# Optimization experiments

Measured on AMD Instinct MI355X. Metric: run time of the kernel, lower is better.

## Reference

```python
import jax, jax.numpy as jnp
import numpy as np

B, N, D, H, E = 4, 1024, 512, 8, 5
HD = D // H  # head_dim = 64


def _xavier(k, shape):
    fan_out, fan_in = shape
    s = (2.0 / (fan_in + fan_out)) ** 0.5
    return jax.random.normal(k, shape, jnp.float32) * s


def setup_inputs() -> dict:
    key = jax.random.key(0)
    ks = jax.random.split(key, 7)
    x = jax.random.normal(ks[0], (B, N, D), jnp.float32)
    edge_features = jax.random.normal(ks[1], (B, N, N, E), jnp.float32)
    node_mask = jax.random.randint(ks[2], (B, N), 0, 2).astype(bool)
    w_qkv = _xavier(ks[3], (3 * D, D))
    w_ep = _xavier(ks[4], (H, E))
    w_eg = _xavier(ks[5], (H, E))
    b_eg = jnp.zeros((H,), jnp.float32)
    w_proj = _xavier(ks[6], (D, D))
    b_proj = jnp.zeros((D,), jnp.float32)
    return {"x": x, "edge_features": edge_features, "node_mask": node_mask,
            "w_qkv": w_qkv, "w_ep": w_ep, "w_eg": w_eg, "b_eg": b_eg,
            "w_proj": w_proj, "b_proj": b_proj}


def reference(x, edge_features, node_mask, w_qkv, w_ep, w_eg, b_eg, w_proj, b_proj):
    b, n, d = x.shape
    scale = HD ** -0.5
    # qkv projection (torch Linear: y = x @ W^T), split into q,k,v (b,H,n,HD)
    qkv = (x @ w_qkv.T).reshape(b, n, 3, H, HD)
    qkv = jnp.transpose(qkv, (2, 0, 3, 1, 4))
    q, k, v = qkv[0], qkv[1], qkv[2]
    # attention scores (b,H,n,n)
    scores = jnp.einsum('bhnd,bhmd->bhnm', q, k) * scale
    # edge bias and sigmoid gate, (b,n,n,E) @ (E,H) -> (b,H,n,n)
    edge_bias = jnp.einsum('bnme,he->bhnm', edge_features, w_ep)
    edge_gates = jax.nn.sigmoid(
        jnp.einsum('bnme,he->bhnm', edge_features, w_eg) + b_eg[None, :, None, None])
    scores = scores + edge_gates * edge_bias
    # pairwise valid mask, broadcast over heads
    m = node_mask[:, None, :, None] & node_mask[:, None, None, :]  # (b,1,n,n)
    scores = jnp.where(m, scores, -jnp.inf)
    row_valid = jnp.any(m, axis=-1)  # (b,1,n)
    scores = jnp.where(row_valid[..., None], scores, 0.0)
    attn = jax.nn.softmax(scores, axis=-1)
    out = jnp.einsum('bhnm,bhmd->bhnd', attn, v)
    out = jnp.transpose(out, (0, 2, 1, 3)).reshape(b, n, d)
    return out @ w_proj.T + b_proj
```

## Files before the change

kernel.cpp:

```cpp
#include <hip/hip_runtime.h>
#include <hip/hip_bf16.h>

#define Bb 4
#define Nn 1024
#define Dd 512
#define Hh 8
#define Ee 5
#define HDd 64

typedef unsigned int u32_t;
typedef unsigned short u16_t;
typedef short s16x8 __attribute__((ext_vector_type(8)));
typedef float f32x4 __attribute__((ext_vector_type(4)));

#define MFMA(a, b, c) __builtin_amdgcn_mfma_f32_16x16x32_bf16((a), (b), (c), 0, 0, 0)

__device__ __forceinline__ void lds_barrier() {
    asm volatile("s_waitcnt lgkmcnt(0)" ::: "memory");
    __builtin_amdgcn_s_barrier();
    asm volatile("" ::: "memory");
}

__device__ __forceinline__ u32_t pack32(float x) {
    u32_t u = __float_as_uint(x);
    u32_t hi = u & 0xffff0000u;
    float rem = x - __uint_as_float(hi);
    u32_t r = __float_as_uint(rem);
    u32_t lo = (r + 0x7fffu + ((r >> 16) & 1u)) >> 16;
    return hi | (lo & 0xffffu);
}

__device__ __forceinline__ void unpk8(uint4 A, uint4 B, s16x8& h, s16x8& l) {
    union { u16_t u[8]; s16x8 v; } H, L;
    u32_t a[8] = {A.x, A.y, A.z, A.w, B.x, B.y, B.z, B.w};
    #pragma unroll
    for (int i = 0; i < 8; i++) { H.u[i] = (u16_t)(a[i] >> 16); L.u[i] = (u16_t)(a[i] & 0xffffu); }
    h = H.v; l = L.v;
}

__device__ __forceinline__ void split4(uint4 A, uint2& hi, uint2& lo) {
    hi.x = (A.x >> 16) | (A.y & 0xffff0000u);
    hi.y = (A.z >> 16) | (A.w & 0xffff0000u);
    lo.x = (A.x & 0xffffu) | (A.y << 16);
    lo.y = (A.z & 0xffffu) | (A.w << 16);
}

__device__ __forceinline__ void stage16(uint4 A0, uint4 A1, uint4 A2, uint4 A3,
                                        u16_t* dh, u16_t* dl) {
    uint2 h0, l0, h1, l1, h2, l2, h3, l3;
    split4(A0, h0, l0); split4(A1, h1, l1); split4(A2, h2, l2); split4(A3, h3, l3);
    *(uint4*)(dh + 0) = make_uint4(h0.x, h0.y, h1.x, h1.y);
    *(uint4*)(dh + 8) = make_uint4(h2.x, h2.y, h3.x, h3.y);
    *(uint4*)(dl + 0) = make_uint4(l0.x, l0.y, l1.x, l1.y);
    *(uint4*)(dl + 8) = make_uint4(l2.x, l2.y, l3.x, l3.y);
}

__global__ __launch_bounds__(256) void pack_prep(const float* __restrict__ x,
                                                 const float* __restrict__ wq,
                                                 const float* __restrict__ wpj,
                                                 const void* __restrict__ msk,
                                                 u32_t* __restrict__ xp,
                                                 u32_t* __restrict__ wqp,
                                                 u32_t* __restrict__ wpp,
                                                 int* __restrict__ mw,
                                                 int* __restrict__ anyB) {
    __shared__ int notint;
    __shared__ int ab[Bb];
    const int tid = threadIdx.x;
    if (blockIdx.x == 1024) {
        if (tid == 0) notint = 0;
        if (tid < Bb) ab[tid] = 0;
        __syncthreads();
        const u32_t* wp = (const u32_t*)msk;
        int bad = 0;
        for (int i = tid; i < 1024; i += 256) bad |= (wp[i] > 1u);
        if (bad) atomicOr(&notint, 1);
        __syncthreads();
        const int isbyte = notint;
        const unsigned char* bp = (const unsigned char*)msk;
        for (int i = tid; i < Bb * Nn; i += 256) {
            const int v = isbyte ? (bp[i] != 0) : (wp[i] != 0);
            mw[i] = v;
            if (v) atomicOr(&ab[i >> 10], 1);
        }
        __syncthreads();
        if (tid < Bb) anyB[tid] = ab[tid];
        return;
    }
    const int gt = blockIdx.x * 256 + tid;
    const int gs = 1024 * 256;
    const float4* xs = (const float4*)x;
    uint4* xd = (uint4*)xp;
    for (int i = gt; i < (Bb * Nn * Dd) / 4; i += gs) {
        float4 v = xs[i];
        xd[i] = make_uint4(pack32(v.x), pack32(v.y), pack32(v.z), pack32(v.w));
    }
    const float4* qs = (const float4*)wq;
    uint4* qd = (uint4*)wqp;
    for (int i = gt; i < (3 * Dd * Dd) / 4; i += gs) {
        float4 v = qs[i];
        qd[i] = make_uint4(pack32(v.x), pack32(v.y), pack32(v.z), pack32(v.w));
    }
    const float4* ps = (const float4*)wpj;
    uint4* pd = (uint4*)wpp;
    for (int i = gt; i < (Dd * Dd) / 4; i += gs) {
        float4 v = ps[i];
        pd[i] = make_uint4(pack32(v.x), pack32(v.y), pack32(v.z), pack32(v.w));
    }
}

__global__ __launch_bounds__(256) void qkv_mfma(const u32_t* __restrict__ xp,
                                                const u32_t* __restrict__ wp,
                                                u32_t* __restrict__ q32,
                                                u32_t* __restrict__ k32,
                                                u32_t* __restrict__ v32) {
    __shared__ __align__(16) u16_t Xh[64 * 72], Xl[64 * 72];
    __shared__ __align__(16) u16_t Wh[64 * 72], Wl[64 * 72];
    const int tid = threadIdx.x;
    const int wv = tid >> 6, lane = tid & 63, lm = lane & 15, quad = lane >> 4;
    const int m0 = blockIdx.y * 64, c0 = blockIdx.x * 64;
    const int row = tid >> 2, dq = tid & 3;
    const uint4* x4 = (const uint4*)xp;
    const uint4* w4 = (const uint4*)wp;

    const size_t xb0 = (size_t)(m0 + row) * 128 + dq * 4;
    const size_t wb0 = (size_t)(c0 + row) * 128 + dq * 4;
    uint4 xa0 = x4[xb0 + 0], xa1 = x4[xb0 + 1], xa2 = x4[xb0 + 2], xa3 = x4[xb0 + 3];
    uint4 wa0 = w4[wb0 + 0], wa1 = w4[wb0 + 1], wa2 = w4[wb0 + 2], wa3 = w4[wb0 + 3];

    f32x4 acc[4];
    #pragma unroll
    for (int nt = 0; nt < 4; nt++) acc[nt] = {0.f, 0.f, 0.f, 0.f};

    for (int kt = 0; kt < 8; kt++) {
        lds_barrier();
        stage16(xa0, xa1, xa2, xa3, &Xh[row * 72 + dq * 16], &Xl[row * 72 + dq * 16]);
        stage16(wa0, wa1, wa2, wa3, &Wh[row * 72 + dq * 16], &Wl[row * 72 + dq * 16]);
        const int ktn = (kt < 7) ? kt + 1 : 7;
        xa0 = x4[xb0 + ktn * 16 + 0]; xa1 = x4[xb0 + ktn * 16 + 1];
        xa2 = x4[xb0 + ktn * 16 + 2]; xa3 = x4[xb0 + ktn * 16 + 3];
        wa0 = w4[wb0 + ktn * 16 + 0]; wa1 = w4[wb0 + ktn * 16 + 1];
        wa2 = w4[wb0 + ktn * 16 + 2]; wa3 = w4[wb0 + ktn * 16 + 3];
        lds_barrier();
        s16x8 ah[2], al[2];
        #pragma unroll
        for (int ks = 0; ks < 2; ks++) {
            ah[ks] = *(const s16x8*)&Xh[(16 * wv + lm) * 72 + ks * 32 + quad * 8];
            al[ks] = *(const s16x8*)&Xl[(16 * wv + lm) * 72 + ks * 32 + quad * 8];
        }
        #pragma unroll
        for (int nt = 0; nt < 4; nt++) {
            #pragma unroll
            for (int ks = 0; ks < 2; ks++) {
                s16x8 bh = *(const s16x8*)&Wh[(16 * nt + lm) * 72 + ks * 32 + quad * 8];
                s16x8 bl = *(const s16x8*)&Wl[(16 * nt + lm) * 72 + ks * 32 + quad * 8];
                acc[nt] = MFMA(ah[ks], bh, acc[nt]);
                acc[nt] = MFMA(ah[ks], bl, acc[nt]);
                acc[nt] = MFMA(al[ks], bh, acc[nt]);
            }
        }
    }
    #pragma unroll
    for (int nt = 0; nt < 4; nt++) {
        const int c = c0 + 16 * nt + lm;
        const int s = c >> 9, hd = c & 511, h = hd >> 6, d = hd & 63;
        u32_t* dst = (s == 0) ? q32 : (s == 1) ? k32 : v32;
        #pragma unroll
        for (int r = 0; r < 4; r++) {
            const int m = m0 + 16 * wv + 4 * quad + r;
            const int b = m >> 10, n = m & (Nn - 1);
            dst[(((size_t)b * Hh + h) * Nn + n) * HDd + d] = pack32(acc[nt][r]);
        }
    }
}

__global__ __launch_bounds__(256, 2) void attn_mfma(const u32_t* __restrict__ q32,
                                                    const u32_t* __restrict__ k32,
                                                    const u32_t* __restrict__ v32,
                                                    const float* __restrict__ ef,
                                                    const int* __restrict__ mw,
                                                    const int* __restrict__ anyB,
                                                    const float* __restrict__ wep,
                                                    const float* __restrict__ weg,
                                                    const float* __restrict__ beg,
                                                    u32_t* __restrict__ aoutp) {
    __shared__ __align__(16) u16_t Qh[64 * 72], Ql[64 * 72];
    __shared__ __align__(16) u16_t Kh[64 * 72], Kl[64 * 72];
    __shared__ __align__(16) u16_t VTh[64 * 88], VTl[64 * 88];
    __shared__ __align__(16) u32_t Ppk[64 * 68];

    const int tid = threadIdx.x;
    const int wv = tid >> 6, lane = tid & 63, lm = lane & 15, quad = lane >> 4;
    const int i0 = blockIdx.x * 64;
    const int h  = blockIdx.y;
    const int b  = blockIdx.z;
    const int row = tid >> 2, dq = tid & 3;
    const int jg = tid >> 4, dc = tid & 15;

    const uint4* qg4 = (const uint4*)(q32 + (((size_t)b * Hh + h) * Nn + i0) * HDd);
    const uint4* kg4 = (const uint4*)(k32 + (((size_t)b * Hh + h) * Nn) * HDd);
    const uint4* vg4 = (const uint4*)(v32 + (((size_t)b * Hh + h) * Nn) * HDd);
    const int* mwB = mw + b * Nn;

    const size_t qb = (size_t)row * 16 + dq * 4;
    uint4 qA0 = qg4[qb + 0], qA1 = qg4[qb + 1], qA2 = qg4[qb + 2], qA3 = qg4[qb + 3];
    uint4 kr0 = kg4[qb + 0], kr1 = kg4[qb + 1], kr2 = kg4[qb + 2], kr3 = kg4[qb + 3];
    uint4 vr0 = vg4[(4 * jg + 0) * 16 + dc], vr1 = vg4[(4 * jg + 1) * 16 + dc],
          vr2 = vg4[(4 * jg + 2) * 16 + dc], vr3 = vg4[(4 * jg + 3) * 16 + dc];

    const int i_sm = i0 + 16 * wv + lm;
    const float* efL = ef + ((size_t)(b * Nn + i_sm) * Nn + 4 * quad) * Ee;
    int4 mj4[4];
    float4 er4[4][5];
    #pragma unroll
    for (int jn = 0; jn < 4; jn++) {
        mj4[jn] = *(const int4*)&mwB[16 * jn + 4 * quad];
        const float4* p4 = (const float4*)(efL + (size_t)(16 * jn) * Ee);
        #pragma unroll
        for (int c = 0; c < 5; c++) er4[jn][c] = p4[c];
    }

    const float wp0 = wep[h*Ee+0], wp1 = wep[h*Ee+1], wp2 = wep[h*Ee+2],
                wp3 = wep[h*Ee+3], wp4 = wep[h*Ee+4];
    const float wg0 = weg[h*Ee+0], wg1 = weg[h*Ee+1], wg2 = weg[h*Ee+2],
                wg3 = weg[h*Ee+3], wg4 = weg[h*Ee+4];
    const float bgs = beg[h];
    const int anyb = anyB[b];
    const int rvs = anyb && mwB[i_sm];

    stage16(qA0, qA1, qA2, qA3, &Qh[row * 72 + dq * 16], &Ql[row * 72 + dq * 16]);
    lds_barrier();
    s16x8 qh[2], ql[2];
    #pragma unroll
    for (int ks = 0; ks < 2; ks++) {
        qh[ks] = *(const s16x8*)&Qh[(16 * wv + lm) * 72 + ks * 32 + quad * 8];
        ql[ks] = *(const s16x8*)&Ql[(16 * wv + lm) * 72 + ks * 32 + quad * 8];
    }

    float m_ = -1e30f, l_ = 0.f;
    f32x4 accO[4];
    #pragma unroll
    for (int dn = 0; dn < 4; dn++) accO[dn] = {0.f, 0.f, 0.f, 0.f};
    const int xk = 8 * (lm & 3);

    for (int jt = 0; jt < Nn / 64; jt++) {
        const int jtn = (jt + 1 < Nn / 64) ? jt + 1 : Nn / 64 - 1;
        const int j0n = jtn * 64;

        lds_barrier();

        stage16(kr0, kr1, kr2, kr3, &Kh[row * 72 + dq * 16], &Kl[row * 72 + dq * 16]);
        {
            u32_t r0[4] = {vr0.x, vr0.y, vr0.z, vr0.w};
            u32_t r1[4] = {vr1.x, vr1.y, vr1.z, vr1.w};
            u32_t r2[4] = {vr2.x, vr2.y, vr2.z, vr2.w};
            u32_t r3[4] = {vr3.x, vr3.y, vr3.z, vr3.w};
            #pragma unroll
            for (int c = 0; c < 4; c++) {
                const int d = 4 * dc + c;
                uint2 hi, lo;
                hi.x = (r0[c] >> 16) | (r1[c] & 0xffff0000u);
                hi.y = (r2[c] >> 16) | (r3[c] & 0xffff0000u);
                lo.x = (r0[c] & 0xffffu) | (r1[c] << 16);
                lo.y = (r2[c] & 0xffffu) | (r3[c] << 16);
                *(uint2*)&VTh[d * 88 + 4 * jg] = hi;
                *(uint2*)&VTl[d * 88 + 4 * jg] = lo;
            }
        }
        {
            const size_t kbn = (size_t)(j0n + row) * 16 + dq * 4;
            kr0 = kg4[kbn + 0]; kr1 = kg4[kbn + 1]; kr2 = kg4[kbn + 2]; kr3 = kg4[kbn + 3];
            vr0 = vg4[(j0n + 4 * jg + 0) * 16 + dc];
            vr1 = vg4[(j0n + 4 * jg + 1) * 16 + dc];
            vr2 = vg4[(j0n + 4 * jg + 2) * 16 + dc];
            vr3 = vg4[(j0n + 4 * jg + 3) * 16 + dc];
        }

        lds_barrier();

        f32x4 Sp[4];
        #pragma unroll
        for (int jn = 0; jn < 4; jn++) {
            f32x4 s = {0.f, 0.f, 0.f, 0.f};
            #pragma unroll
            for (int ks = 0; ks < 2; ks++) {
                s16x8 kh = *(const s16x8*)&Kh[(16 * jn + lm) * 72 + ks * 32 + quad * 8];
                s16x8 kl = *(const s16x8*)&Kl[(16 * jn + lm) * 72 + ks * 32 + quad * 8];
                s = MFMA(kh, qh[ks], s);
                s = MFMA(kh, ql[ks], s);
                s = MFMA(kl, qh[ks], s);
            }
            Sp[jn] = s;
        }

        float pp[4][4];
        #pragma unroll
        for (int jn = 0; jn < 4; jn++) {
            const int mjv[4] = {mj4[jn].x, mj4[jn].y, mj4[jn].z, mj4[jn].w};
            #pragma unroll
            for (int r = 0; r < 4; r++) {
                const int f = r * 5;
                const float e0 = er4[jn][(f+0)>>2][(f+0)&3];
                const float e1 = er4[jn][(f+1)>>2][(f+1)&3];
                const float e2 = er4[jn][(f+2)>>2][(f+2)&3];
                const float e3 = er4[jn][(f+3)>>2][(f+3)&3];
                const float e4 = er4[jn][(f+4)>>2][(f+4)&3];
                const float bias = fmaf(e0, wp0, fmaf(e1, wp1, fmaf(e2, wp2, fmaf(e3, wp3, e4 * wp4))));
                const float gv = fmaf(e0, wg0, fmaf(e1, wg1, fmaf(e2, wg2, fmaf(e3, wg3, fmaf(e4, wg4, bgs)))));
                const float gate = __builtin_amdgcn_rcpf(1.f + __expf(-gv));
                const float val = fmaf(Sp[jn][r], 0.125f, gate * bias);
                pp[jn][r] = rvs ? (mjv[r] ? val : -1e30f) : 0.f;
            }
        }
        #pragma unroll
        for (int jn = 0; jn < 4; jn++) {
            mj4[jn] = *(const int4*)&mwB[j0n + 16 * jn + 4 * quad];
            const float4* p4 = (const float4*)(efL + (size_t)(j0n + 16 * jn) * Ee);
            #pragma unroll
            for (int c = 0; c < 5; c++) er4[jn][c] = p4[c];
        }

        float tmax = fmaxf(fmaxf(fmaxf(pp[0][0], pp[0][1]), fmaxf(pp[0][2], pp[0][3])),
                           fmaxf(fmaxf(pp[1][0], pp[1][1]), fmaxf(pp[1][2], pp[1][3])));
        tmax = fmaxf(tmax,
               fmaxf(fmaxf(fmaxf(pp[2][0], pp[2][1]), fmaxf(pp[2][2], pp[2][3])),
                     fmaxf(fmaxf(pp[3][0], pp[3][1]), fmaxf(pp[3][2], pp[3][3]))));
        tmax = fmaxf(tmax, __shfl_xor(tmax, 16));
        tmax = fmaxf(tmax, __shfl_xor(tmax, 32));
        const float mnew = fmaxf(m_, tmax);
        const float alpha = __expf(m_ - mnew);
        float ps = 0.f;
        #pragma unroll
        for (int jn = 0; jn < 4; jn++)
            #pragma unroll
            for (int r = 0; r < 4; r++) { pp[jn][r] = __expf(pp[jn][r] - mnew); ps += pp[jn][r]; }
        ps += __shfl_xor(ps, 16);
        ps += __shfl_xor(ps, 32);
        m_ = mnew;
        l_ = l_ * alpha + ps;
        float a4[4];
        #pragma unroll
        for (int r = 0; r < 4; r++) a4[r] = __shfl(alpha, 4 * quad + r);
        #pragma unroll
        for (int dn = 0; dn < 4; dn++)
            #pragma unroll
            for (int r = 0; r < 4; r++) accO[dn][r] *= a4[r];

        #pragma unroll
        for (int jn = 0; jn < 4; jn++) {
            #pragma unroll
            for (int p = 0; p < 2; p++) {
                const int col = (16 * jn + 4 * quad + 2 * p) ^ xk;
                *(uint2*)&Ppk[(16 * wv + lm) * 68 + col] =
                    make_uint2(pack32(pp[jn][2 * p]), pack32(pp[jn][2 * p + 1]));
            }
        }

        s16x8 ph[2], pl[2];
        #pragma unroll
        for (int ks2 = 0; ks2 < 2; ks2++) {
            const int off = (16 * wv + lm) * 68 + ((ks2 * 32 + quad * 8) ^ xk);
            uint4 A = *(const uint4*)&Ppk[off];
            uint4 B2 = *(const uint4*)&Ppk[off + 4];
            unpk8(A, B2, ph[ks2], pl[ks2]);
        }
        #pragma unroll
        for (int dn = 0; dn < 4; dn++) {
            f32x4 c = accO[dn];
            #pragma unroll
            for (int ks2 = 0; ks2 < 2; ks2++) {
                s16x8 vh = *(const s16x8*)&VTh[(16 * dn + lm) * 88 + ks2 * 32 + quad * 8];
                s16x8 vl = *(const s16x8*)&VTl[(16 * dn + lm) * 88 + ks2 * 32 + quad * 8];
                c = MFMA(ph[ks2], vh, c);
                c = MFMA(ph[ks2], vl, c);
                c = MFMA(pl[ks2], vh, c);
            }
            accO[dn] = c;
        }
    }

    float linv[4];
    #pragma unroll
    for (int r = 0; r < 4; r++) linv[r] = __builtin_amdgcn_rcpf(__shfl(l_, 4 * quad + r));
    #pragma unroll
    for (int r = 0; r < 4; r++) {
        const int i = i0 + 16 * wv + 4 * quad + r;
        #pragma unroll
        for (int dn = 0; dn < 4; dn++)
            aoutp[(size_t)(b * Nn + i) * Dd + h * HDd + 16 * dn + lm] = pack32(accO[dn][r] * linv[r]);
    }
}

__global__ __launch_bounds__(256) void out_mfma(const u32_t* __restrict__ ap,
                                                const u32_t* __restrict__ wp,
                                                const float* __restrict__ bias,
                                                float* __restrict__ out) {
    __shared__ __align__(16) u16_t Xh[64 * 72], Xl[64 * 72];
    __shared__ __align__(16) u16_t Wh[64 * 72], Wl[64 * 72];
    const int tid = threadIdx.x;
    const int wv = tid >> 6, lane = tid & 63, lm = lane & 15, quad = lane >> 4;
    const int m0 = blockIdx.y * 64, c0 = blockIdx.x * 64;
    const int row = tid >> 2, dq = tid & 3;
    const uint4* a4 = (const uint4*)ap;
    const uint4* w4 = (const uint4*)wp;

    const size_t ab0 = (size_t)(m0 + row) * 128 + dq * 4;
    const size_t wb0 = (size_t)(c0 + row) * 128 + dq * 4;
    uint4 xa0 = a4[ab0 + 0], xa1 = a4[ab0 + 1], xa2 = a4[ab0 + 2], xa3 = a4[ab0 + 3];
    uint4 wa0 = w4[wb0 + 0], wa1 = w4[wb0 + 1], wa2 = w4[wb0 + 2], wa3 = w4[wb0 + 3];

    f32x4 acc[4];
    #pragma unroll
    for (int nt = 0; nt < 4; nt++) acc[nt] = {0.f, 0.f, 0.f, 0.f};

    for (int kt = 0; kt < 8; kt++) {
        lds_barrier();
        stage16(xa0, xa1, xa2, xa3, &Xh[row * 72 + dq * 16], &Xl[row * 72 + dq * 16]);
        stage16(wa0, wa1, wa2, wa3, &Wh[row * 72 + dq * 16], &Wl[row * 72 + dq * 16]);
        const int ktn = (kt < 7) ? kt + 1 : 7;
        xa0 = a4[ab0 + ktn * 16 + 0]; xa1 = a4[ab0 + ktn * 16 + 1];
        xa2 = a4[ab0 + ktn * 16 + 2]; xa3 = a4[ab0 + ktn * 16 + 3];
        wa0 = w4[wb0 + ktn * 16 + 0]; wa1 = w4[wb0 + ktn * 16 + 1];
        wa2 = w4[wb0 + ktn * 16 + 2]; wa3 = w4[wb0 + ktn * 16 + 3];
        lds_barrier();
        s16x8 ah[2], al[2];
        #pragma unroll
        for (int ks = 0; ks < 2; ks++) {
            ah[ks] = *(const s16x8*)&Xh[(16 * wv + lm) * 72 + ks * 32 + quad * 8];
            al[ks] = *(const s16x8*)&Xl[(16 * wv + lm) * 72 + ks * 32 + quad * 8];
        }
        #pragma unroll
        for (int nt = 0; nt < 4; nt++) {
            #pragma unroll
            for (int ks = 0; ks < 2; ks++) {
                s16x8 bh = *(const s16x8*)&Wh[(16 * nt + lm) * 72 + ks * 32 + quad * 8];
                s16x8 bl = *(const s16x8*)&Wl[(16 * nt + lm) * 72 + ks * 32 + quad * 8];
                acc[nt] = MFMA(ah[ks], bh, acc[nt]);
                acc[nt] = MFMA(ah[ks], bl, acc[nt]);
                acc[nt] = MFMA(al[ks], bh, acc[nt]);
            }
        }
    }
    #pragma unroll
    for (int nt = 0; nt < 4; nt++) {
        const int c = c0 + 16 * nt + lm;
        const float bc = bias[c];
        #pragma unroll
        for (int r = 0; r < 4; r++) {
            const int m = m0 + 16 * wv + 4 * quad + r;
            out[(size_t)m * Dd + c] = acc[nt][r] + bc;
        }
    }
}

extern "C" void kernel_launch(void* const* d_in, const int* in_sizes, int n_in,
                              void* d_out, int out_size, void* d_ws, size_t ws_size,
                              hipStream_t stream) {
    const float* x    = (const float*)d_in[0];
    const float* ef   = (const float*)d_in[1];
    const void*  msk  = d_in[2];
    const float* wqkv = (const float*)d_in[3];
    const float* wep  = (const float*)d_in[4];
    const float* weg  = (const float*)d_in[5];
    const float* beg  = (const float*)d_in[6];
    const float* wpj  = (const float*)d_in[7];
    const float* bpj  = (const float*)d_in[8];
    float* out = (float*)d_out;

    int* mw   = (int*)d_ws;
    int* anyB = mw + Bb * Nn;
    u32_t* q32 = (u32_t*)(anyB + 16);
    const size_t per = (size_t)Bb * Hh * Nn * HDd;
    u32_t* k32 = q32 + per;
    u32_t* v32 = k32 + per;
    u32_t* aop = v32 + per;
    u32_t* xp  = aop + (size_t)Bb * Nn * Dd;
    u32_t* wqp = xp + (size_t)Bb * Nn * Dd;
    u32_t* wpp = wqp + (size_t)3 * Dd * Dd;

    pack_prep<<<1025, 256, 0, stream>>>(x, wqkv, wpj, msk, xp, wqp, wpp, mw, anyB);
    qkv_mfma<<<dim3(24, 64), 256, 0, stream>>>(xp, wqp, q32, k32, v32);
    attn_mfma<<<dim3(Nn / 64, Hh, Bb), 256, 0, stream>>>(q32, k32, v32, ef, mw, anyB,
                                                         wep, weg, beg, aop);
    out_mfma<<<dim3(8, 64), 256, 0, stream>>>(aop, wpp, bpj, out);
}
```

Baseline: 310.8 us.

## Bit-pack node mask, load Q directly to registers, widen V transpose stores

The node mask is packed into 32-bit bitmasks, so the attention kernel reads one uint2 per tile instead of four int4 loads per lane. The Q tile no longer goes through LDS: each lane loads its own Q row fragment and splits it into hi/lo bf16 halves in registers, which removes the Qh/Ql shared arrays and a barrier. The V transpose staging now gathers 8 rows with uint2 loads and writes 16-byte vectors to LDS instead of 8-byte ones. These changes cut LDS footprint and memory traffic at the cost of more uncoalesced per-lane Q loads and extra registers.

```diff
diff --git a/kernel.cpp b/kernel.cpp
--- a/kernel.cpp
+++ b/kernel.cpp
@@ -55,6 +55,9 @@
     *(uint4*)(dl + 8) = make_uint4(l2.x, l2.y, l3.x, l3.y);
 }
 
+#define HHW(a, b) (((a) >> 16) | ((b) & 0xffff0000u))
+#define LLW(a, b) (((a) & 0xffffu) | ((b) << 16))
+
 __global__ __launch_bounds__(256) void pack_prep(const float* __restrict__ x,
                                                  const float* __restrict__ wq,
                                                  const float* __restrict__ wpj,
@@ -62,7 +65,7 @@
                                                  u32_t* __restrict__ xp,
                                                  u32_t* __restrict__ wqp,
                                                  u32_t* __restrict__ wpp,
-                                                 int* __restrict__ mw,
+                                                 u32_t* __restrict__ mb,
                                                  int* __restrict__ anyB) {
     __shared__ int notint;
     __shared__ int ab[Bb];
@@ -78,10 +81,15 @@
         __syncthreads();
         const int isbyte = notint;
         const unsigned char* bp = (const unsigned char*)msk;
-        for (int i = tid; i < Bb * Nn; i += 256) {
-            const int v = isbyte ? (bp[i] != 0) : (wp[i] != 0);
-            mw[i] = v;
-            if (v) atomicOr(&ab[i >> 10], 1);
+        if (tid < 128) {
+            u32_t wbits = 0;
+            for (int k = 0; k < 32; k++) {
+                const int i = tid * 32 + k;
+                const int v = isbyte ? (bp[i] != 0) : (wp[i] != 0);
+                wbits |= (u32_t)v << k;
+            }
+            mb[tid] = wbits;
+            if (wbits) atomicOr(&ab[tid >> 5], 1);
         }
         __syncthreads();
         if (tid < Bb) anyB[tid] = ab[tid];
@@ -178,13 +186,12 @@
                                                     const u32_t* __restrict__ k32,
                                                     const u32_t* __restrict__ v32,
                                                     const float* __restrict__ ef,
-                                                    const int* __restrict__ mw,
+                                                    const u32_t* __restrict__ mb,
                                                     const int* __restrict__ anyB,
                                                     const float* __restrict__ wep,
                                                     const float* __restrict__ weg,
                                                     const float* __restrict__ beg,
                                                     u32_t* __restrict__ aoutp) {
-    __shared__ __align__(16) u16_t Qh[64 * 72], Ql[64 * 72];
     __shared__ __align__(16) u16_t Kh[64 * 72], Kl[64 * 72];
     __shared__ __align__(16) u16_t VTh[64 * 88], VTl[64 * 88];
     __shared__ __align__(16) u32_t Ppk[64 * 68];
@@ -195,26 +202,31 @@
     const int h  = blockIdx.y;
     const int b  = blockIdx.z;
     const int row = tid >> 2, dq = tid & 3;
-    const int jg = tid >> 4, dc = tid & 15;
-
-    const uint4* qg4 = (const uint4*)(q32 + (((size_t)b * Hh + h) * Nn + i0) * HDd);
+    const int jo = tid >> 5, dch = tid & 31;
+
     const uint4* kg4 = (const uint4*)(k32 + (((size_t)b * Hh + h) * Nn) * HDd);
-    const uint4* vg4 = (const uint4*)(v32 + (((size_t)b * Hh + h) * Nn) * HDd);
-    const int* mwB = mw + b * Nn;
-
-    const size_t qb = (size_t)row * 16 + dq * 4;
-    uint4 qA0 = qg4[qb + 0], qA1 = qg4[qb + 1], qA2 = qg4[qb + 2], qA3 = qg4[qb + 3];
-    uint4 kr0 = kg4[qb + 0], kr1 = kg4[qb + 1], kr2 = kg4[qb + 2], kr3 = kg4[qb + 3];
-    uint4 vr0 = vg4[(4 * jg + 0) * 16 + dc], vr1 = vg4[(4 * jg + 1) * 16 + dc],
-          vr2 = vg4[(4 * jg + 2) * 16 + dc], vr3 = vg4[(4 * jg + 3) * 16 + dc];
+    const uint2* vg2 = (const uint2*)(v32 + (((size_t)b * Hh + h) * Nn) * HDd);
+    const u32_t* mbB = mb + b * 32;
 
     const int i_sm = i0 + 16 * wv + lm;
+
+    const u32_t* qrow = q32 + (((size_t)b * Hh + h) * Nn + i_sm) * HDd;
+    uint4 qA0 = *(const uint4*)&qrow[quad * 8];
+    uint4 qB0 = *(const uint4*)&qrow[quad * 8 + 4];
+    uint4 qA1 = *(const uint4*)&qrow[32 + quad * 8];
+    uint4 qB1 = *(const uint4*)&qrow[32 + quad * 8 + 4];
+    const size_t kb0 = (size_t)row * 16 + dq * 4;
+    uint4 kr0 = kg4[kb0 + 0], kr1 = kg4[kb0 + 1], kr2 = kg4[kb0 + 2], kr3 = kg4[kb0 + 3];
+    uint2 vq0 = vg2[(8 * jo + 0) * 32 + dch], vq1 = vg2[(8 * jo + 1) * 32 + dch],
+          vq2 = vg2[(8 * jo + 2) * 32 + dch], vq3 = vg2[(8 * jo + 3) * 32 + dch],
+          vq4 = vg2[(8 * jo + 4) * 32 + dch], vq5 = vg2[(8 * jo + 5) * 32 + dch],
+          vq6 = vg2[(8 * jo + 6) * 32 + dch], vq7 = vg2[(8 * jo + 7) * 32 + dch];
+
     const float* efL = ef + ((size_t)(b * Nn + i_sm) * Nn + 4 * quad) * Ee;
-    int4 mj4[4];
+    uint2 mwc = *(const uint2*)&mbB[0];
     float4 er4[4][5];
     #pragma unroll
     for (int jn = 0; jn < 4; jn++) {
-        mj4[jn] = *(const int4*)&mwB[16 * jn + 4 * quad];
         const float4* p4 = (const float4*)(efL + (size_t)(16 * jn) * Ee);
         #pragma unroll
         for (int c = 0; c < 5; c++) er4[jn][c] = p4[c];
@@ -226,16 +238,11 @@
                 wg3 = weg[h*Ee+3], wg4 = weg[h*Ee+4];
     const float bgs = beg[h];
     const int anyb = anyB[b];
-    const int rvs = anyb && mwB[i_sm];
-
-    stage16(qA0, qA1, qA2, qA3, &Qh[row * 72 + dq * 16], &Ql[row * 72 + dq * 16]);
-    lds_barrier();
+    const int rvs = anyb && ((mbB[i_sm >> 5] >> (i_sm & 31)) & 1);
+
     s16x8 qh[2], ql[2];
-    #pragma unroll
-    for (int ks = 0; ks < 2; ks++) {
-        qh[ks] = *(const s16x8*)&Qh[(16 * wv + lm) * 72 + ks * 32 + quad * 8];
-        ql[ks] = *(const s16x8*)&Ql[(16 * wv + lm) * 72 + ks * 32 + quad * 8];
-    }
+    unpk8(qA0, qB0, qh[0], ql[0]);
+    unpk8(qA1, qB1, qh[1], ql[1]);
 
     float m_ = -1e30f, l_ = 0.f;
     f32x4 accO[4];
@@ -251,29 +258,31 @@
 
         stage16(kr0, kr1, kr2, kr3, &Kh[row * 72 + dq * 16], &Kl[row * 72 + dq * 16]);
         {
-            u32_t r0[4] = {vr0.x, vr0.y, vr0.z, vr0.w};
-            u32_t r1[4] = {vr1.x, vr1.y, vr1.z, vr1.w};
-            u32_t r2[4] = {vr2.x, vr2.y, vr2.z, vr2.w};
-            u32_t r3[4] = {vr3.x, vr3.y, vr3.z, vr3.w};
-            #pragma unroll
-            for (int c = 0; c < 4; c++) {
-                const int d = 4 * dc + c;
-                uint2 hi, lo;
-                hi.x = (r0[c] >> 16) | (r1[c] & 0xffff0000u);
-                hi.y = (r2[c] >> 16) | (r3[c] & 0xffff0000u);
-                lo.x = (r0[c] & 0xffffu) | (r1[c] << 16);
-                lo.y = (r2[c] & 0xffffu) | (r3[c] << 16);
-                *(uint2*)&VTh[d * 88 + 4 * jg] = hi;
-                *(uint2*)&VTl[d * 88 + 4 * jg] = lo;
-            }
+            const int d0 = 2 * dch, d1 = d0 + 1;
+            uint4 H0 = make_uint4(HHW(vq0.x, vq1.x), HHW(vq2.x, vq3.x),
+                                  HHW(vq4.x, vq5.x), HHW(vq6.x, vq7.x));
+            uint4 L0 = make_uint4(LLW(vq0.x, vq1.x), LLW(vq2.x, vq3.x),
+                                  LLW(vq4.x, vq5.x), LLW(vq6.x, vq7.x));
+            uint4 H1 = make_uint4(HHW(vq0.y, vq1.y), HHW(vq2.y, vq3.y),
+                                  HHW(vq4.y, vq5.y), HHW(vq6.y, vq7.y));
+            uint4 L1 = make_uint4(LLW(vq0.y, vq1.y), LLW(vq2.y, vq3.y),
+                                  LLW(vq4.y, vq5.y), LLW(vq6.y, vq7.y));
+            *(uint4*)&VTh[d0 * 88 + 8 * jo] = H0;
+            *(uint4*)&VTl[d0 * 88 + 8 * jo] = L0;
+            *(uint4*)&VTh[d1 * 88 + 8 * jo] = H1;
+            *(uint4*)&VTl[d1 * 88 + 8 * jo] = L1;
         }
         {
             const size_t kbn = (size_t)(j0n + row) * 16 + dq * 4;
             kr0 = kg4[kbn + 0]; kr1 = kg4[kbn + 1]; kr2 = kg4[kbn + 2]; kr3 = kg4[kbn + 3];
-            vr0 = vg4[(j0n + 4 * jg + 0) * 16 + dc];
-            vr1 = vg4[(j0n + 4 * jg + 1) * 16 + dc];
-            vr2 = vg4[(j0n + 4 * jg + 2) * 16 + dc];
-            vr3 = vg4[(j0n + 4 * jg + 3) * 16 + dc];
+            vq0 = vg2[(j0n + 8 * jo + 0) * 32 + dch];
+            vq1 = vg2[(j0n + 8 * jo + 1) * 32 + dch];
+            vq2 = vg2[(j0n + 8 * jo + 2) * 32 + dch];
+            vq3 = vg2[(j0n + 8 * jo + 3) * 32 + dch];
+            vq4 = vg2[(j0n + 8 * jo + 4) * 32 + dch];
+            vq5 = vg2[(j0n + 8 * jo + 5) * 32 + dch];
+            vq6 = vg2[(j0n + 8 * jo + 6) * 32 + dch];
+            vq7 = vg2[(j0n + 8 * jo + 7) * 32 + dch];
         }
 
         lds_barrier();
@@ -293,12 +302,15 @@
             Sp[jn] = s;
         }
 
+        const u32_t sj0 = mwc.x >> (4 * quad), sj1 = mwc.x >> (4 * quad + 16);
+        const u32_t sj2 = mwc.y >> (4 * quad), sj3 = mwc.y >> (4 * quad + 16);
+        const u32_t sj[4] = {sj0, sj1, sj2, sj3};
         float pp[4][4];
         #pragma unroll
         for (int jn = 0; jn < 4; jn++) {
-            const int mjv[4] = {mj4[jn].x, mj4[jn].y, mj4[jn].z, mj4[jn].w};
             #pragma unroll
             for (int r = 0; r < 4; r++) {
+                const int mjv = (sj[jn] >> r) & 1;
                 const int f = r * 5;
                 const float e0 = er4[jn][(f+0)>>2][(f+0)&3];
                 const float e1 = er4[jn][(f+1)>>2][(f+1)&3];
@@ -309,12 +321,12 @@
                 const float gv = fmaf(e0, wg0, fmaf(e1, wg1, fmaf(e2, wg2, fmaf(e3, wg3, fmaf(e4, wg4, bgs)))));
                 const float gate = __builtin_amdgcn_rcpf(1.f + __expf(-gv));
                 const float val = fmaf(Sp[jn][r], 0.125f, gate * bias);
-                pp[jn][r] = rvs ? (mjv[r] ? val : -1e30f) : 0.f;
-            }
-        }
+                pp[jn][r] = rvs ? (mjv ? val : -1e30f) : 0.f;
+            }
+        }
+        mwc = *(const uint2*)&mbB[j0n >> 5];
         #pragma unroll
         for (int jn = 0; jn < 4; jn++) {
-            mj4[jn] = *(const int4*)&mwB[j0n + 16 * jn + 4 * quad];
             const float4* p4 = (const float4*)(efL + (size_t)(j0n + 16 * jn) * Ee);
             #pragma unroll
             for (int c = 0; c < 5; c++) er4[jn][c] = p4[c];
@@ -467,8 +479,8 @@
     const float* bpj  = (const float*)d_in[8];
     float* out = (float*)d_out;
 
-    int* mw   = (int*)d_ws;
-    int* anyB = mw + Bb * Nn;
+    u32_t* mbits = (u32_t*)d_ws;
+    int* anyB = (int*)(mbits + 128);
     u32_t* q32 = (u32_t*)(anyB + 16);
     const size_t per = (size_t)Bb * Hh * Nn * HDd;
     u32_t* k32 = q32 + per;
@@ -478,9 +490,9 @@
     u32_t* wqp = xp + (size_t)Bb * Nn * Dd;
     u32_t* wpp = wqp + (size_t)3 * Dd * Dd;
 
-    pack_prep<<<1025, 256, 0, stream>>>(x, wqkv, wpj, msk, xp, wqp, wpp, mw, anyB);
+    pack_prep<<<1025, 256, 0, stream>>>(x, wqkv, wpj, msk, xp, wqp, wpp, mbits, anyB);
     qkv_mfma<<<dim3(24, 64), 256, 0, stream>>>(xp, wqp, q32, k32, v32);
-    attn_mfma<<<dim3(Nn / 64, Hh, Bb), 256, 0, stream>>>(q32, k32, v32, ef, mw, anyB,
+    attn_mfma<<<dim3(Nn / 64, Hh, Bb), 256, 0, stream>>>(q32, k32, v32, ef, mbits, anyB,
                                                          wep, weg, beg, aop);
     out_mfma<<<dim3(8, 64), 256, 0, stream>>>(aop, wpp, bpj, out);
 }
```

After: 300.1 us. -3.4%, faster.
